# Kernel optimization log

Hardware: AMD Instinct MI355X
Metric: run time of the kernel (lower is better)

## Reference

```python
import jax, jax.numpy as jnp
import numpy as np

B = 8192
EPS = 1e-5  # BatchNorm eps (torch default)


def binarize(x):
    # sign binarization with straight-through estimator (matches the .data trick
    # in BinarizeConv2d/BinarizeLinear: forward sees +-1, backward sees identity)
    s = jnp.where(x >= 0, 1.0, -1.0).astype(x.dtype)
    return x + jax.lax.stop_gradient(s - x)


def conv2d(x, w, stride, pad):
    return jax.lax.conv_general_dilated(
        x, w, window_strides=stride, padding=pad,
        dimension_numbers=('NCHW', 'OIHW', 'NCHW'))


def bn(x, g, b, m, v):
    # eval-mode BatchNorm2d folded into one scale+shift per channel
    inv = g * jax.lax.rsqrt(v + EPS)
    return x * inv[None, :, None, None] + (b - m * inv)[None, :, None, None]


def maxpool_w2(x):
    # MaxPool2d(kernel=(1,2), stride=(1,2))
    return jax.lax.reduce_window(x, -jnp.inf, jax.lax.max,
                                 (1, 1, 1, 2), (1, 1, 1, 2), 'VALID')


def setup_inputs() -> dict:
    key = jax.random.key(0)
    ks = jax.random.split(key, 32)
    d = {}
    d['x'] = jax.random.normal(ks[0], (B, 1, 6, 128), jnp.float32)

    def w(k, shape):
        return jax.random.normal(k, shape, jnp.float32) * 0.05

    # conv weights (OIHW) and biases
    d['w1'] = w(ks[1], (32, 1, 1, 9));    d['b1'] = w(ks[2], (32,))
    d['w2'] = w(ks[3], (64, 32, 1, 3));   d['b2'] = w(ks[4], (64,))
    d['w3'] = w(ks[5], (128, 64, 1, 3));  d['b3'] = w(ks[6], (128,))
    d['w4'] = w(ks[7], (128, 128, 6, 1)); d['b4'] = w(ks[8], (128,))
    # BatchNorm params (gamma, beta, running_mean, running_var)
    for i, c in zip((1, 2, 3, 4), (32, 64, 128, 128)):
        kk = jax.random.split(ks[8 + i], 4)
        d[f'g{i}'] = 1.0 + 0.1 * jax.random.normal(kk[0], (c,), jnp.float32)
        d[f'be{i}'] = 0.1 * jax.random.normal(kk[1], (c,), jnp.float32)
        d[f'm{i}'] = 0.1 * jax.random.normal(kk[2], (c,), jnp.float32)
        d[f'v{i}'] = jax.random.uniform(kk[3], (c,), jnp.float32, 0.5, 1.5)
    # fc: BinarizeLinear(2048, 10)
    d['wf'] = w(ks[20], (10, 2048))
    d['bf'] = w(ks[21], (10,))
    return d


def reference(x, w1, b1, w2, b2, w3, b3, w4, b4,
              g1, be1, m1, v1, g2, be2, m2, v2,
              g3, be3, m3, v3, g4, be4, m4, v4, wf, bf):
    # block 1: first layer keeps real-valued input, binarized weights
    h = conv2d(x, binarize(w1), (1, 2), [(0, 0), (4, 4)]) + b1[None, :, None, None]
    h = jnp.clip(bn(h, g1, be1, m1, v1), -1.0, 1.0)   # Hardtanh
    h = maxpool_w2(h)                                  # [B,32,6,32]
    # block 2: binarized activations + weights
    h = conv2d(binarize(h), binarize(w2), (1, 1), [(0, 0), (1, 1)]) + b2[None, :, None, None]
    h = jnp.clip(bn(h, g2, be2, m2, v2), -1.0, 1.0)    # [B,64,6,32]
    # block 3
    h = conv2d(binarize(h), binarize(w3), (1, 1), [(0, 0), (1, 1)]) + b3[None, :, None, None]
    h = jnp.clip(bn(h, g3, be3, m3, v3), -1.0, 1.0)
    h = maxpool_w2(h)                                  # [B,128,6,16]
    # block 4: (6,1) kernel collapses H
    h = conv2d(binarize(h), binarize(w4), (1, 1), [(0, 0), (0, 0)]) + b4[None, :, None, None]
    h = jnp.clip(bn(h, g4, be4, m4, v4), -1.0, 1.0)    # [B,128,1,16]
    h = h.reshape(h.shape[0], -1)                      # [B,2048]
    return binarize(h) @ binarize(wf).T + bf           # [B,10]
```

## Files before the change

### kernel.cpp

```cpp
#include <hip/hip_runtime.h>
#include <cstdint>
#include <cstddef>
#include <math.h>

#define BATCH 8192

typedef unsigned long long u64;
typedef uint32_t u32;
typedef int v4i __attribute__((ext_vector_type(4)));
typedef int v16i __attribute__((ext_vector_type(16)));

__device__ __forceinline__ double bn_inv_d(float g, float v) {
    return (double)g * (1.0 / sqrt((double)v + 1e-5));
}
__device__ __forceinline__ double bn_shift_d(float be, float m, double iv) {
    return (double)be - (double)m * iv;
}
__device__ __forceinline__ double bn_eval_d(double conv, double B, double iv, double sh) {
    return (conv + B) * iv + sh;
}

__global__ __launch_bounds__(256) void prep_all(
    const float* w1, const float* b1, const float* w2, const float* b2,
    const float* w3, const float* b3, const float* w4, const float* b4,
    const float* wf,
    const float* g1, const float* be1, const float* m1, const float* v1,
    const float* g2, const float* be2, const float* m2, const float* v2,
    const float* g3, const float* be3, const float* m3, const float* v3,
    const float* g4, const float* be4, const float* m4, const float* v4,
    float* s1f, double* T1, u32* wt2w, int* T2,
    uint4* b3i8, int* C3, u64* wt4, int* T4, u64* wtf) {
    int t = blockIdx.x * 256 + threadIdx.x;

    if (t < 384) {
        int co = t / 12, k = t % 12;
        float val = 0.f;
        if (k < 9) {
            double iv = bn_inv_d(g1[co], v1[co]);
            float d = (iv < 0.0) ? -1.f : 1.f;
            val = ((w1[co * 9 + k] >= 0.f) ? 1.f : -1.f) * d;
        }
        s1f[t] = val;
    } else if (t < 416) {
        int co = t - 384;
        double iv = bn_inv_d(g1[co], v1[co]);
        double sh = bn_shift_d(be1[co], m1[co], iv);
        double B = (double)b1[co];
        bool flip = (iv < 0.0);
        double tt = -sh / iv - B;
        T1[co] = flip ? -tt : tt;
    } else if (t < 608) {
        int idx = t - 416;
        int co = idx / 3, kw = idx % 3;
        double iv = bn_inv_d(g2[co], v2[co]);
        bool flip = (iv < 0.0);
        u32 wb = 0;
        for (int ci = 0; ci < 32; ++ci)
            wb |= (u32)((w2[(co * 32 + ci) * 3 + kw] >= 0.f) != flip) << ci;
        wt2w[co * 4 + kw] = wb;
    } else if (t < 800) {
        int idx = t - 608;
        int co = idx & 63, cls = idx >> 6;
        double iv = bn_inv_d(g2[co], v2[co]);
        double sh = bn_shift_d(be2[co], m2[co], iv);
        double B = (double)b2[co];
        bool flip = (iv < 0.0);
        int spur = 0, nv = 3;
        if (cls == 1) { nv = 2; for (int ci = 0; ci < 32; ++ci) spur += (int)((w2[(co * 32 + ci) * 3 + 0] >= 0.f) != flip); }
        if (cls == 2) { nv = 2; for (int ci = 0; ci < 32; ++ci) spur += (int)((w2[(co * 32 + ci) * 3 + 2] >= 0.f) != flip); }
        int maxp = 32 * nv + spur;
        int T = -1;
        for (int p = 0; p <= maxp; ++p) {
            int conv = flip ? (2 * (p - spur) - 32 * nv) : (32 * nv - 2 * (p - spur));
            double y = bn_eval_d((double)conv, B, iv, sh);
            if ((y >= 0.0) && (T == p - 1)) T = p;
        }
        T2[cls * 64 + co] = T;
    } else if (t < 2336) {
        int idx = t - 800;
        int q = idx >> 7, n = idx & 127;
        double iv = bn_inv_d(g3[n], v3[n]);
        bool flip = (iv < 0.0);
        int kw = q >> 2, ci0 = (q & 3) * 16;
        u32 wd[4] = {0, 0, 0, 0};
        for (int j = 0; j < 16; ++j) {
            int ci = ci0 + j;
            bool pos = (w3[(n * 64 + ci) * 3 + kw] >= 0.f) != flip;
            u32 byte = pos ? 0x01u : 0xFFu;
            wd[j >> 2] |= byte << (8 * (j & 3));
        }
        b3i8[idx] = make_uint4(wd[0], wd[1], wd[2], wd[3]);
    } else if (t < 2464) {
        int co = t - 2336;
        double iv = bn_inv_d(g3[co], v3[co]);
        double sh = bn_shift_d(be3[co], m3[co], iv);
        double B = (double)b3[co];
        int C = 1000;
        if (iv >= 0.0) {
            for (int v = -192; v <= 192; v += 2)
                if (bn_eval_d((double)v, B, iv, sh) >= 0.0) { C = v; break; }
        } else {
            for (int v = 192; v >= -192; v -= 2)
                if (bn_eval_d((double)v, B, iv, sh) >= 0.0) { C = -v; break; }
        }
        C3[co] = C;
    } else if (t < 4000) {
        int idx = t - 2464;
        int j = idx & 1, ch = idx >> 1;
        int co = ch / 6, h = ch % 6;
        double iv = bn_inv_d(g4[co], v4[co]);
        bool flip = (iv < 0.0);
        u64 wb = 0;
        for (int cb = 0; cb < 64; ++cb) {
            int ci = j * 64 + cb;
            wb |= (u64)((w4[(co * 128 + ci) * 6 + h] >= 0.f) != flip) << cb;
        }
        wt4[idx] = wb;
    } else if (t < 4128) {
        int co = t - 4000;
        double iv = bn_inv_d(g4[co], v4[co]);
        double sh = bn_shift_d(be4[co], m4[co], iv);
        double B = (double)b4[co];
        bool flip = (iv < 0.0);
        int T = -1;
        for (int p = 0; p <= 768; ++p) {
            int conv = flip ? (2 * p - 768) : (768 - 2 * p);
            double y = bn_eval_d((double)conv, B, iv, sh);
            if ((y >= 0.0) && (T == p - 1)) T = p;
        }
        T4[co] = T;
    } else if (t < 4448) {
        int idx = t - 4128;
        int o = idx / 32, wi = idx % 32;
        u64 wb = 0;
        for (int fb = 0; fb < 64; ++fb)
            wb |= (u64)(wf[o * 2048 + wi * 64 + fb] >= 0.f) << fb;
        wtf[idx] = wb;
    }
}

#define RB 24
__global__ __launch_bounds__(256, 3) void mega_kernel(
    const float* __restrict__ x, const float4* __restrict__ s1p, const double* __restrict__ T1g,
    const uint4* __restrict__ wt2v, const int* __restrict__ T2g,
    const uint4* __restrict__ b3i8, const int* __restrict__ C3g,
    const u64* __restrict__ wt4, const int* __restrict__ T4g,
    const u64* __restrict__ wtf, const float* __restrict__ bfg,
    float* __restrict__ out) {
    __shared__ __attribute__((aligned(16))) char smem[40576];
    uint4* sB3 = (uint4*)smem;
    u64*  sLUT = (u64*)(smem + 24576);
    short* sC3 = (short*)(smem + 26624);
    uint4* sW2 = (uint4*)(smem + 26880);
    short* sT2 = (short*)(smem + 27904);
    float* sX  = (float*)(smem + 28288);
    u32*  sA1  = (u32*)(smem + 32768);
    u64*  sA2  = (u64*)(smem + 34432);
    u64*  sW4  = (u64*)smem;
    u64*  sWf  = (u64*)(smem + 12288);
    u64*  sFeat = (u64*)(smem + 26880);
    short* sT4 = (short*)(smem + 27904);
    float* sBf = (float*)(smem + 28160);
    u32*  sA3u = (u32*)(smem + 28288);
    u64*  sA3q = (u64*)(smem + 28288);

    int t = threadIdx.x;
    for (int i = t; i < 1536; i += 256) sB3[i] = b3i8[i];
    {
        u32 b = t & 255;
        u64 e = 0;
#pragma unroll
        for (int j = 0; j < 8; ++j)
            e |= (((b >> j) & 1) ? 0x01ull : 0xFFull) << (8 * j);
        if (t < 256) sLUT[t] = e;
    }
    if (t < 128) sC3[t] = (short)C3g[t];
    if (t < 64) sW2[t] = wt2v[t];
    if (t < 192) sT2[t] = (short)T2g[t];

    int co = t & 31, lane = t & 63;
    float4 wa = s1p[co * 3 + 0];
    float4 wb = s1p[co * 3 + 1];
    float wc = s1p[co * 3 + 2].x;
    double w0d = (double)wa.x, w1d = (double)wa.y, w2d = (double)wa.z, w3d = (double)wa.w;
    double w4d = (double)wb.x, w5d = (double)wb.y, w6d = (double)wb.z, w7d = (double)wb.w;
    double w8d = (double)wc;
    double Tt = T1g[co];
    float Ttf = (float)Tt;

    int bh0 = blockIdx.x * RB;
#pragma unroll 1
    for (int ch = 0; ch < 3; ++ch) {
        __syncthreads();
        for (int i = t; i < 8 * 140; i += 256) {
            int r = i / 140, c = i % 140;
            float v = 0.f;
            if (c >= 4 && c < 132) v = x[(size_t)(bh0 + ch * 8 + r) * 128 + (c - 4)];
            sX[r * 140 + c] = v;
        }
        __syncthreads();
        {
            int rr = t >> 5;
            const float* xr = &sX[rr * 140];
            float4 A0 = *(const float4*)&xr[0];
            float4 A1 = *(const float4*)&xr[4];
            float4 A2 = *(const float4*)&xr[8];
            u32 myword = 0;
#pragma unroll
            for (int wp = 0; wp < 32; ++wp) {
                float s0 = 0.f, s1 = 0.f;
                s0 = fmaf(wa.x, A0.x, s0);  s1 = fmaf(wa.x, A0.z, s1);
                s0 = fmaf(wa.y, A0.y, s0);  s1 = fmaf(wa.y, A0.w, s1);
                s0 = fmaf(wa.z, A0.z, s0);  s1 = fmaf(wa.z, A1.x, s1);
                s0 = fmaf(wa.w, A0.w, s0);  s1 = fmaf(wa.w, A1.y, s1);
                s0 = fmaf(wb.x, A1.x, s0);  s1 = fmaf(wb.x, A1.z, s1);
                s0 = fmaf(wb.y, A1.y, s0);  s1 = fmaf(wb.y, A1.w, s1);
                s0 = fmaf(wb.z, A1.z, s0);  s1 = fmaf(wb.z, A2.x, s1);
                s0 = fmaf(wb.w, A1.w, s0);  s1 = fmaf(wb.w, A2.y, s1);
                s0 = fmaf(wc,   A2.x, s0);  s1 = fmaf(wc,   A2.z, s1);
                float m0 = fmaxf(s0, s1);
                bool pred = m0 >= Ttf;
                if (__any(fabsf(m0 - Ttf) <= 2e-4f)) {
                    double d0 = 0.0, d1 = 0.0;
                    d0 = fma(w0d, (double)A0.x, d0);  d1 = fma(w0d, (double)A0.z, d1);
                    d0 = fma(w1d, (double)A0.y, d0);  d1 = fma(w1d, (double)A0.w, d1);
                    d0 = fma(w2d, (double)A0.z, d0);  d1 = fma(w2d, (double)A1.x, d1);
                    d0 = fma(w3d, (double)A0.w, d0);  d1 = fma(w3d, (double)A1.y, d1);
                    d0 = fma(w4d, (double)A1.x, d0);  d1 = fma(w4d, (double)A1.z, d1);
                    d0 = fma(w5d, (double)A1.y, d0);  d1 = fma(w5d, (double)A1.w, d1);
                    d0 = fma(w6d, (double)A1.z, d0);  d1 = fma(w6d, (double)A2.x, d1);
                    d0 = fma(w7d, (double)A1.w, d0);  d1 = fma(w7d, (double)A2.y, d1);
                    d0 = fma(w8d, (double)A2.x, d0);  d1 = fma(w8d, (double)A2.z, d1);
                    pred = ((d0 > d1) ? d0 : d1) >= Tt;
                }
                u64 mk = __ballot(pred);
                u32 hw = (lane < 32) ? (u32)mk : (u32)(mk >> 32);
                if ((lane & 31) == wp) myword = hw;
                A0 = A1; A1 = A2;
                A2 = *(const float4*)&xr[4 * wp + 12];
            }
            sA1[(((t >> 6) << 1) + (lane >> 5)) * 32 + (lane & 31)] = myword;
        }
        __syncthreads();
        {
            int r = t >> 5, wp = t & 31;
            u32 am = sA1[r * 32 + wp];
            u32 al = (wp > 0) ? sA1[r * 32 + wp - 1] : 0u;
            u32 ar = (wp < 31) ? sA1[r * 32 + wp + 1] : 0u;
            const short* Tp = &sT2[(wp == 0) ? 64 : ((wp == 31) ? 128 : 0)];
            u64 word2 = 0;
#pragma unroll
            for (int c = 0; c < 64; ++c) {
                uint4 w2v = sW2[c];
                int p = __popc(al ^ w2v.x) + __popc(am ^ w2v.y) + __popc(ar ^ w2v.z);
                word2 |= (u64)(p <= (int)Tp[c]) << c;
            }
            sA2[(ch * 8 + r) * 32 + wp] = word2;
        }
    }
    __syncthreads();

    int wq = t >> 6, m = lane & 31, half = lane >> 5;
    const int prTab[8] = {0, 1, 4, 5, 8, 9, 12, 13};
    for (int r6 = 0; r6 < 6; ++r6) {
        int row = wq * 6 + r6;
        u64 aw = sA2[row * 32 + m];
        u64 wm1 = (m > 0) ? sA2[row * 32 + m - 1] : 0ull;
        u64 wp1 = (m < 31) ? sA2[row * 32 + m + 1] : 0ull;

        v4i A[6];
#pragma unroll
        for (int kk = 0; kk < 6; ++kk) {
            const int kw = kk >> 1;
            u64 word = (kw == 0) ? wm1 : ((kw == 1) ? aw : wp1);
            bool valid = !((kw == 0 && m == 0) || (kw == 2 && m == 31));
            int ci0 = ((kk & 1) << 5) + (half << 4);
            u32 bits = (u32)(word >> ci0) & 0xFFFFu;
            u64 lo = sLUT[bits & 0xFF];
            u64 hi = sLUT[bits >> 8];
            if (!valid) { lo = 0; hi = 0; }
            union { u64 q[2]; v4i v; } u;
            u.q[0] = lo; u.q[1] = hi;
            A[kk] = u.v;
        }
        u32 outv = 0;
#pragma unroll
        for (int nt = 0; nt < 4; ++nt) {
            v16i acc;
#pragma unroll
            for (int i = 0; i < 16; ++i) acc[i] = 0;
#pragma unroll
            for (int kk = 0; kk < 6; ++kk) {
                int q = kk * 2 + half;
                union { uint4 u4; v4i v; } bu;
                bu.u4 = sB3[q * 128 + nt * 32 + m];
                acc = __builtin_amdgcn_mfma_i32_32x32x32_i8(A[kk], bu.v, acc, 0, 0, 0);
            }
            int tc = (int)sC3[nt * 32 + m];
#pragma unroll
            for (int rp = 0; rp < 8; ++rp) {
                bool c = (acc[2 * rp] >= tc) || (acc[2 * rp + 1] >= tc);
                u64 mk = __ballot(c);
                int LA = (nt << 4) | prTab[rp];
                int LB = LA + 2;
                outv = (lane == LA) ? (u32)mk : outv;
                outv = (lane == LB) ? (u32)(mk >> 32) : outv;
            }
        }
        sA3u[row * 64 + ((lane & 15) << 2) + (lane >> 4)] = outv;
    }
    __syncthreads();

    for (int i = t; i < 1536; i += 256) sW4[i] = wt4[i];
    for (int i = t; i < 320; i += 256) sWf[i] = wtf[i];
    if (t < 128) sT4[t] = (short)T4g[t];
    if (t < 10) sBf[t] = bfg[t];
    __syncthreads();

    {
        int bb = t >> 6;
        int w = lane & 15;
        int cg = lane >> 4;
        u64 av[12];
#pragma unroll
        for (int h = 0; h < 6; ++h) {
            av[h * 2 + 0] = sA3q[(bb * 6 + h) * 32 + w * 2 + 0];
            av[h * 2 + 1] = sA3q[(bb * 6 + h) * 32 + w * 2 + 1];
        }
        u64 acc = 0;
#pragma unroll 4
        for (int c = 0; c < 32; ++c) {
            int cc = cg * 32 + c;
            const u64* wr = &sW4[cc * 12];
            int p = 0;
#pragma unroll
            for (int q = 0; q < 12; ++q) p += __popcll(av[q] ^ wr[q]);
            u64 mk = __ballot(p <= (int)sT4[cc]);
            u64 field = (mk >> (cg * 16)) & 0xFFFFull;
            acc |= field << ((c & 3) << 4);
            if ((c & 3) == 3) {
                if (w == (c >> 2)) sFeat[bb * 32 + cg * 8 + (c >> 2)] = acc;
                acc = 0;
            }
        }
    }
    __syncthreads();
    if (t < 40) {
        int fb = t / 10, o = t % 10;
        int p = 0;
#pragma unroll
        for (int wi = 0; wi < 32; ++wi) p += __popcll(sFeat[fb * 32 + wi] ^ sWf[o * 32 + wi]);
        out[(size_t)(blockIdx.x * 4 + fb) * 10 + o] = __fadd_rn((float)(2048 - 2 * p), sBf[o]);
    }
}

extern "C" void kernel_launch(void* const* d_in, const int* in_sizes, int n_in,
                              void* d_out, int out_size, void* d_ws, size_t ws_size,
                              hipStream_t stream) {
    const float* x  = (const float*)d_in[0];
    const float* w1 = (const float*)d_in[1];  const float* b1 = (const float*)d_in[2];
    const float* w2 = (const float*)d_in[3];  const float* b2 = (const float*)d_in[4];
    const float* w3 = (const float*)d_in[5];  const float* b3 = (const float*)d_in[6];
    const float* w4 = (const float*)d_in[7];  const float* b4 = (const float*)d_in[8];
    const float* g1 = (const float*)d_in[9];  const float* be1 = (const float*)d_in[10];
    const float* m1 = (const float*)d_in[11]; const float* v1 = (const float*)d_in[12];
    const float* g2 = (const float*)d_in[13]; const float* be2 = (const float*)d_in[14];
    const float* m2 = (const float*)d_in[15]; const float* v2 = (const float*)d_in[16];
    const float* g3 = (const float*)d_in[17]; const float* be3 = (const float*)d_in[18];
    const float* m3 = (const float*)d_in[19]; const float* v3 = (const float*)d_in[20];
    const float* g4 = (const float*)d_in[21]; const float* be4 = (const float*)d_in[22];
    const float* m4 = (const float*)d_in[23]; const float* v4 = (const float*)d_in[24];
    const float* wf = (const float*)d_in[25]; const float* bf = (const float*)d_in[26];
    float* out = (float*)d_out;

    char* ws = (char*)d_ws;
    uint4*  b3i8 = (uint4*) (ws + 0);
    u64*    wt4  = (u64*)   (ws + 24576);
    u64*    wtf  = (u64*)   (ws + 36864);
    u32*    wt2w = (u32*)   (ws + 39424);
    float*  s1f  = (float*) (ws + 40448);
    double* T1   = (double*)(ws + 41984);
    int*    T2   = (int*)   (ws + 42240);
    int*    C3   = (int*)   (ws + 43008);
    int*    T4   = (int*)   (ws + 43520);

    prep_all<<<18, 256, 0, stream>>>(w1, b1, w2, b2, w3, b3, w4, b4, wf,
                                     g1, be1, m1, v1, g2, be2, m2, v2,
                                     g3, be3, m3, v3, g4, be4, m4, v4,
                                     s1f, T1, wt2w, T2, b3i8, C3, wt4, T4, wtf);

    mega_kernel<<<(BATCH * 6) / RB, 256, 0, stream>>>(
        x, (const float4*)s1f, T1, (const uint4*)wt2w, T2, b3i8, C3,
        wt4, T4, wtf, bf, out);
}
```

Measured before the change: 271.8 us.

## Shrink LDS footprint with nibble LUT, vectorize input staging, raise occupancy

Replaces the 256-entry 64-bit byte-expansion LUT with a 16-entry 32-bit nibble LUT (duplicated per half-wave), which shrinks shared memory enough to raise launch bounds from 3 to 4 blocks per CU. The input row staging now uses float4 global loads instead of scalar loads. The tolerance for the double-precision fallback in layer 1 is tightened, so the slow path is taken less often. In exchange, each A-fragment build does four LDS lookups instead of two, register pressure is tighter at the higher occupancy target, and the narrower tolerance risks sign mismatches near the threshold.

```diff
diff --git a/kernel.cpp b/kernel.cpp
--- a/kernel.cpp
+++ b/kernel.cpp
@@ -140,39 +140,40 @@
 }
 
 #define RB 24
-__global__ __launch_bounds__(256, 3) void mega_kernel(
+__global__ __launch_bounds__(256, 4) void mega_kernel(
     const float* __restrict__ x, const float4* __restrict__ s1p, const double* __restrict__ T1g,
     const uint4* __restrict__ wt2v, const int* __restrict__ T2g,
     const uint4* __restrict__ b3i8, const int* __restrict__ C3g,
     const u64* __restrict__ wt4, const int* __restrict__ T4g,
     const u64* __restrict__ wtf, const float* __restrict__ bfg,
     float* __restrict__ out) {
-    __shared__ __attribute__((aligned(16))) char smem[40576];
-    uint4* sB3 = (uint4*)smem;
-    u64*  sLUT = (u64*)(smem + 24576);
-    short* sC3 = (short*)(smem + 26624);
-    uint4* sW2 = (uint4*)(smem + 26880);
-    short* sT2 = (short*)(smem + 27904);
-    float* sX  = (float*)(smem + 28288);
-    u32*  sA1  = (u32*)(smem + 32768);
-    u64*  sA2  = (u64*)(smem + 34432);
-    u64*  sW4  = (u64*)smem;
-    u64*  sWf  = (u64*)(smem + 12288);
-    u64*  sFeat = (u64*)(smem + 26880);
-    short* sT4 = (short*)(smem + 27904);
-    float* sBf = (float*)(smem + 28160);
-    u32*  sA3u = (u32*)(smem + 28288);
-    u64*  sA3q = (u64*)(smem + 28288);
+    __shared__ __attribute__((aligned(16))) char smem[38656];
+    uint4* sB3  = (uint4*)smem;
+    u32*  sLUT4 = (u32*)(smem + 24576);
+    short* sC3  = (short*)(smem + 24704);
+    uint4* sW2  = (uint4*)(smem + 24960);
+    short* sT2  = (short*)(smem + 25984);
+    float* sX   = (float*)(smem + 26368);
+    u32*  sA1   = (u32*)(smem + 31872 - 1024 + 1024);
+    u64*  sA2   = (u64*)(smem + 32512);
+    sA1 = (u32*)(smem + 30848);
+    u64*  sW4   = (u64*)smem;
+    u64*  sWf   = (u64*)(smem + 12288);
+    u64*  sFeat = (u64*)(smem + 24960);
+    short* sT4  = (short*)(smem + 25984);
+    float* sBf  = (float*)(smem + 26240);
+    u32*  sA3u  = (u32*)(smem + 26368);
+    u64*  sA3q  = (u64*)(smem + 26368);
 
     int t = threadIdx.x;
     for (int i = t; i < 1536; i += 256) sB3[i] = b3i8[i];
-    {
-        u32 b = t & 255;
-        u64 e = 0;
-#pragma unroll
-        for (int j = 0; j < 8; ++j)
-            e |= (((b >> j) & 1) ? 0x01ull : 0xFFull) << (8 * j);
-        if (t < 256) sLUT[t] = e;
+    if (t < 32) {
+        u32 n = t & 15;
+        u32 e = 0;
+#pragma unroll
+        for (int j = 0; j < 4; ++j)
+            e |= (((n >> j) & 1) ? 0x01u : 0xFFu) << (8 * j);
+        sLUT4[t] = e;
     }
     if (t < 128) sC3[t] = (short)C3g[t];
     if (t < 64) sW2[t] = wt2v[t];
@@ -192,11 +193,12 @@
 #pragma unroll 1
     for (int ch = 0; ch < 3; ++ch) {
         __syncthreads();
-        for (int i = t; i < 8 * 140; i += 256) {
-            int r = i / 140, c = i % 140;
-            float v = 0.f;
-            if (c >= 4 && c < 132) v = x[(size_t)(bh0 + ch * 8 + r) * 128 + (c - 4)];
-            sX[r * 140 + c] = v;
+        for (int i = t; i < 280; i += 256) {
+            int r = i / 35, c = i - r * 35;
+            float4 v = make_float4(0.f, 0.f, 0.f, 0.f);
+            if (c >= 1 && c <= 32)
+                v = *(const float4*)&x[(size_t)(bh0 + ch * 8 + r) * 128 + (c * 4 - 4)];
+            *(float4*)&sX[r * 140 + c * 4] = v;
         }
         __syncthreads();
         {
@@ -220,7 +222,7 @@
                 s0 = fmaf(wc,   A2.x, s0);  s1 = fmaf(wc,   A2.z, s1);
                 float m0 = fmaxf(s0, s1);
                 bool pred = m0 >= Ttf;
-                if (__any(fabsf(m0 - Ttf) <= 2e-4f)) {
+                if (__any(fabsf(m0 - Ttf) <= 5e-5f)) {
                     double d0 = 0.0, d1 = 0.0;
                     d0 = fma(w0d, (double)A0.x, d0);  d1 = fma(w0d, (double)A0.z, d1);
                     d0 = fma(w1d, (double)A0.y, d0);  d1 = fma(w1d, (double)A0.w, d1);
@@ -261,6 +263,7 @@
     __syncthreads();
 
     int wq = t >> 6, m = lane & 31, half = lane >> 5;
+    const u32* lp = sLUT4 + (half << 4);
     const int prTab[8] = {0, 1, 4, 5, 8, 9, 12, 13};
     for (int r6 = 0; r6 < 6; ++r6) {
         int row = wq * 6 + r6;
@@ -276,11 +279,13 @@
             bool valid = !((kw == 0 && m == 0) || (kw == 2 && m == 31));
             int ci0 = ((kk & 1) << 5) + (half << 4);
             u32 bits = (u32)(word >> ci0) & 0xFFFFu;
-            u64 lo = sLUT[bits & 0xFF];
-            u64 hi = sLUT[bits >> 8];
-            if (!valid) { lo = 0; hi = 0; }
-            union { u64 q[2]; v4i v; } u;
-            u.q[0] = lo; u.q[1] = hi;
+            u32 b0 = lp[bits & 15];
+            u32 b1 = lp[(bits >> 4) & 15];
+            u32 b2 = lp[(bits >> 8) & 15];
+            u32 b3v = lp[bits >> 12];
+            if (!valid) { b0 = 0; b1 = 0; b2 = 0; b3v = 0; }
+            union { u32 d[4]; v4i v; } u;
+            u.d[0] = b0; u.d[1] = b1; u.d[2] = b2; u.d[3] = b3v;
             A[kk] = u.v;
         }
         u32 outv = 0;
```

New measurement: 266.9 us. About the same (-1.8%).
